# Optimization experiments

Measured on AMD Instinct MI355X. Metric: run time of the kernel, lower is better.

The kernel has to match this reference:

```python
import jax, jax.numpy as jnp
import numpy as np

B, T, F_IN, F_OUT = 16, 2048, 128, 128
ALPHA = 0.2  # LeakyReLU negative slope
MASK_VAL = -1e9


def setup_inputs() -> dict:
    key = jax.random.key(0)
    kx, kw, ka, kadj = jax.random.split(key, 4)
    # xavier_uniform-ish scale for W and a (gain=1.414)
    w_bound = 1.414 * np.sqrt(6.0 / (F_IN + F_OUT))
    a_bound = 1.414 * np.sqrt(6.0 / (2 * F_OUT + 1))
    x = jax.random.normal(kx, (B, T, F_IN), jnp.float32)
    W = jax.random.uniform(kw, (F_IN, F_OUT), jnp.float32, -w_bound, w_bound)
    a = jax.random.uniform(ka, (2 * F_OUT, 1), jnp.float32, -a_bound, a_bound)
    adj = jax.random.randint(kadj, (B, T, T), 0, 2, jnp.int32)
    return {"x": x, "adj": adj, "W": W, "a": a}


def reference(x, adj, W, a):
    # h: [B,T,F_OUT]
    h = jnp.einsum('btf,fo->bto', x, W)
    # Additive GAT score decomposition: e[b,i,j] = leakyrelu(h_i . a1 + h_j . a2)
    # Mathematically identical to cat([h_i,h_j]) @ a, without the BxTxTx2F tensor.
    a1 = a[:F_OUT, 0]   # [F_OUT]
    a2 = a[F_OUT:, 0]   # [F_OUT]
    s1 = h @ a1         # [B,T]
    s2 = h @ a2         # [B,T]
    e = jax.nn.leaky_relu(s1[:, :, None] + s2[:, None, :], ALPHA)  # [B,T,T]
    e = jnp.where(adj == 0, MASK_VAL, e)
    att = jax.nn.softmax(e, axis=-1)  # [B,T,T]
    # dropout=0.0 / eval mode -> identity
    return att @ h  # [B,T,F_OUT]
```

## Files before the change

kernel.cpp:

```cpp
#include <hip/hip_runtime.h>

#define TT 2048
#define NB 16
#define FD 128
#define ALPHA 0.2f

typedef __attribute__((ext_vector_type(8))) short short8;
typedef __attribute__((ext_vector_type(4))) float f32x4;

static __device__ __forceinline__ unsigned short f2bf(float f) {
    unsigned u = __float_as_uint(f);
    u += 0x7FFF + ((u >> 16) & 1);
    return (unsigned short)(u >> 16);
}
static __device__ __forceinline__ float bf2f(unsigned short s) {
    return __uint_as_float(((unsigned)s) << 16);
}

__global__ __launch_bounds__(256) void k_wt(const float* __restrict__ W,
                                            unsigned short* __restrict__ WT)
{
    int fid = blockIdx.x * 256 + threadIdx.x;
    int k = fid >> 5;
    int f = (fid & 31) << 2;
    float4 w4 = *reinterpret_cast<const float4*>(W + k * FD + f);
    WT[(f + 0) * FD + k] = f2bf(w4.x);
    WT[(f + 1) * FD + k] = f2bf(w4.y);
    WT[(f + 2) * FD + k] = f2bf(w4.z);
    WT[(f + 3) * FD + k] = f2bf(w4.w);
}

__global__ __launch_bounds__(256) void k_h(const float* __restrict__ x,
                                           const unsigned short* __restrict__ WT,
                                           const float* __restrict__ a,
                                           unsigned short* __restrict__ hT,
                                           float* __restrict__ s1,
                                           float* __restrict__ s2)
{
    __shared__ unsigned short hs[128][72];

    const int tid = threadIdx.x;
    const int b  = blockIdx.x >> 5;
    const int t0 = (blockIdx.x & 31) << 6;
    const int w = tid >> 6, l = tid & 63, g = l >> 4, r15 = l & 15;

    const float* xrow = x + ((size_t)(b * TT + t0 + w * 16 + r15)) * FD;

    f32x4 acc[8] = {};

    #pragma unroll
    for (int m = 0; m < 4; ++m) {
        const int koff = m * 32 + g * 8;
        float4 xa = *reinterpret_cast<const float4*>(xrow + koff);
        float4 xb = *reinterpret_cast<const float4*>(xrow + koff + 4);
        short8 af;
        af[0] = (short)f2bf(xa.x); af[1] = (short)f2bf(xa.y);
        af[2] = (short)f2bf(xa.z); af[3] = (short)f2bf(xa.w);
        af[4] = (short)f2bf(xb.x); af[5] = (short)f2bf(xb.y);
        af[6] = (short)f2bf(xb.z); af[7] = (short)f2bf(xb.w);
        #pragma unroll
        for (int n = 0; n < 8; ++n) {
            short8 bfr = *reinterpret_cast<const short8*>(WT + (n * 16 + r15) * FD + koff);
            acc[n] = __builtin_amdgcn_mfma_f32_16x16x32_bf16(af, bfr, acc[n], 0, 0, 0);
        }
    }

    float p1[4] = {0.f, 0.f, 0.f, 0.f}, p2[4] = {0.f, 0.f, 0.f, 0.f};
    #pragma unroll
    for (int n = 0; n < 8; ++n) {
        float a1v = a[n * 16 + r15];
        float a2v = a[FD + n * 16 + r15];
        #pragma unroll
        for (int r = 0; r < 4; ++r) {
            p1[r] += acc[n][r] * a1v;
            p2[r] += acc[n][r] * a2v;
        }
    }
    #pragma unroll
    for (int r = 0; r < 4; ++r) {
        #pragma unroll
        for (int off = 8; off >= 1; off >>= 1) {
            p1[r] += __shfl_xor(p1[r], off);
            p2[r] += __shfl_xor(p2[r], off);
        }
    }
    if (r15 == 0) {
        const int trow = t0 + w * 16 + g * 4;
        #pragma unroll
        for (int r = 0; r < 4; ++r) {
            s1[b * TT + trow + r] = p1[r];
            s2[b * TT + trow + r] = p2[r];
        }
    }

    #pragma unroll
    for (int n = 0; n < 8; ++n)
        #pragma unroll
        for (int r = 0; r < 4; ++r)
            hs[n * 16 + r15][w * 16 + g * 4 + r] = f2bf(acc[n][r]);
    __syncthreads();

    for (int i = tid; i < 1024; i += 256) {
        int f = i >> 3, c = i & 7;
        short8 v = *reinterpret_cast<const short8*>(&hs[f][c * 8]);
        *reinterpret_cast<short8*>(hT + ((size_t)(b * FD + f)) * TT + t0 + c * 8) = v;
    }
}

__global__ __launch_bounds__(256) void k_att(const int* __restrict__ adj,
                                             const unsigned short* __restrict__ hT,
                                             const float* __restrict__ s1,
                                             const float* __restrict__ s2,
                                             float* __restrict__ out)
{
    __shared__ __align__(16) unsigned short pbuf[2][32][136];
    __shared__ float dsum[32];

    const int tid = threadIdx.x;
    const int wg = (blockIdx.x & 7) * 128 + (blockIdx.x >> 3);
    const int b  = wg >> 6;
    const int i0 = (wg & 63) << 5;
    const int w = tid >> 6, l = tid & 63, g = l >> 4, r15 = l & 15;

    const int pr = tid >> 3;
    const int cg = tid & 7;
    const int* adjp = adj + ((size_t)(b * TT + i0 + pr)) * TT + cg * 16;
    const float s1v = s1[b * TT + i0 + pr];
    const float* s2p = s2 + b * TT + cg * 16;
    unsigned short* prow = &pbuf[0][pr][cg * 16];

    const int f0 = w * 32;
    const unsigned short* hB0 = hT + (size_t)b * FD * TT + (size_t)(f0 + r15) * TT;
    const unsigned short* hB1 = hB0 + (size_t)(16 * TT);

    f32x4 acc00 = {}, acc01 = {}, acc10 = {}, acc11 = {};
    float rsum = 0.f;

    int4 arA[4], arB[4];
    #pragma unroll
    for (int q = 0; q < 4; ++q)
        arA[q] = *reinterpret_cast<const int4*>(adjp + q * 4);

    auto body = [&](int t, int4 (&cur)[4], int4 (&nxt)[4], const int bsel) {
        const int j0 = t * 128;
        if (t < 15) {
            #pragma unroll
            for (int q = 0; q < 4; ++q)
                nxt[q] = *reinterpret_cast<const int4*>(adjp + j0 + 128 + q * 4);
        }
        float4 s2v[4];
        #pragma unroll
        for (int q = 0; q < 4; ++q)
            s2v[q] = *reinterpret_cast<const float4*>(s2p + j0 + q * 4);
        short8 v0, v1;
        const int*   cai = (const int*)cur;
        const float* csf = (const float*)s2v;
        #pragma unroll
        for (int e = 0; e < 16; ++e) {
            float s = s1v + csf[e];
            s = fmaxf(s, ALPHA * s);
            float p = cai[e] ? __expf(s) : 0.f;
            unsigned short u = f2bf(p);
            rsum += bf2f(u);
            if (e < 8) v0[e] = (short)u; else v1[e - 8] = (short)u;
        }
        unsigned short* dst = prow + bsel * (32 * 136);
        *reinterpret_cast<short8*>(dst)     = v0;
        *reinterpret_cast<short8*>(dst + 8) = v1;
        asm volatile("s_waitcnt lgkmcnt(0)" ::: "memory");
        __builtin_amdgcn_s_barrier();
        asm volatile("" ::: "memory");
        const unsigned short* pb = &pbuf[bsel][0][0];
        #pragma unroll
        for (int kk = 0; kk < 4; ++kk) {
            short8 A0 = *reinterpret_cast<const short8*>(pb + r15 * 136 + kk * 32 + g * 8);
            short8 A1 = *reinterpret_cast<const short8*>(pb + (16 + r15) * 136 + kk * 32 + g * 8);
            short8 B0 = *reinterpret_cast<const short8*>(hB0 + j0 + kk * 32 + g * 8);
            short8 B1 = *reinterpret_cast<const short8*>(hB1 + j0 + kk * 32 + g * 8);
            acc00 = __builtin_amdgcn_mfma_f32_16x16x32_bf16(A0, B0, acc00, 0, 0, 0);
            acc01 = __builtin_amdgcn_mfma_f32_16x16x32_bf16(A0, B1, acc01, 0, 0, 0);
            acc10 = __builtin_amdgcn_mfma_f32_16x16x32_bf16(A1, B0, acc10, 0, 0, 0);
            acc11 = __builtin_amdgcn_mfma_f32_16x16x32_bf16(A1, B1, acc11, 0, 0, 0);
        }
    };

    for (int tt = 0; tt < 8; ++tt) {
        body(2 * tt,     arA, arB, 0);
        body(2 * tt + 1, arB, arA, 1);
    }

    rsum += __shfl_xor(rsum, 1);
    rsum += __shfl_xor(rsum, 2);
    rsum += __shfl_xor(rsum, 4);
    if ((tid & 7) == 0) dsum[pr] = rsum;
    __syncthreads();

    float rinv0[4], rinv1[4];
    #pragma unroll
    for (int r = 0; r < 4; ++r) {
        rinv0[r] = 1.0f / dsum[g * 4 + r];
        rinv1[r] = 1.0f / dsum[16 + g * 4 + r];
    }
    const size_t obase = ((size_t)(b * TT + i0)) * FD + f0 + r15;
    #pragma unroll
    for (int r = 0; r < 4; ++r) {
        float* o0 = out + obase + (size_t)(g * 4 + r) * FD;
        float* o1 = out + obase + (size_t)(16 + g * 4 + r) * FD;
        o0[0]  = acc00[r] * rinv0[r];
        o0[16] = acc01[r] * rinv0[r];
        o1[0]  = acc10[r] * rinv1[r];
        o1[16] = acc11[r] * rinv1[r];
    }
}

extern "C" void kernel_launch(void* const* d_in, const int* in_sizes, int n_in,
                              void* d_out, int out_size, void* d_ws, size_t ws_size,
                              hipStream_t stream)
{
    const float* x  = (const float*)d_in[0];
    const int* adj  = (const int*)d_in[1];
    const float* W  = (const float*)d_in[2];
    const float* a  = (const float*)d_in[3];
    float* out = (float*)d_out;

    unsigned short* hT = (unsigned short*)d_ws;
    float* s1 = (float*)((char*)d_ws + (size_t)NB * FD * TT * 2);
    float* s2 = s1 + NB * TT;
    unsigned short* WT = (unsigned short*)(s2 + NB * TT);

    k_wt <<<16, 256, 0, stream>>>(W, WT);
    k_h  <<<NB * (TT / 64), 256, 0, stream>>>(x, WT, a, hT, s1, s2);
    k_att<<<NB * (TT / 32), 256, 0, stream>>>(adj, hT, s1, s2, out);
}
```

Before: 123.4 us.

## Shrink attention row tile from 32 to 16 rows to double block count

The attention kernel now handles 16 query rows per block instead of 32, launching twice as many blocks with half the accumulators and half the shared-memory P buffer, and adds an occupancy hint of 8 blocks per CU. Each thread computes 8 probabilities per 128-column step instead of 16. This is meant to raise parallelism and occupancy so the adjacency stream, which dominates traffic, is fetched with more memory-level parallelism. The cost is that the hT tile is read from global/L2 twice as many times in total, and MFMA work per barrier is halved.

```diff
diff --git a/kernel.cpp b/kernel.cpp
--- a/kernel.cpp
+++ b/kernel.cpp
@@ -107,66 +107,60 @@
     }
 }
 
-__global__ __launch_bounds__(256) void k_att(const int* __restrict__ adj,
-                                             const unsigned short* __restrict__ hT,
-                                             const float* __restrict__ s1,
-                                             const float* __restrict__ s2,
-                                             float* __restrict__ out)
-{
-    __shared__ __align__(16) unsigned short pbuf[2][32][136];
-    __shared__ float dsum[32];
+__global__ __launch_bounds__(256, 8) void k_att(const int* __restrict__ adj,
+                                                const unsigned short* __restrict__ hT,
+                                                const float* __restrict__ s1,
+                                                const float* __restrict__ s2,
+                                                float* __restrict__ out)
+{
+    __shared__ __align__(16) unsigned short pbuf[2][16][136];
+    __shared__ float dsum[16];
 
     const int tid = threadIdx.x;
-    const int wg = (blockIdx.x & 7) * 128 + (blockIdx.x >> 3);
-    const int b  = wg >> 6;
-    const int i0 = (wg & 63) << 5;
+    const int wg = (blockIdx.x & 7) * 256 + (blockIdx.x >> 3);
+    const int b  = wg >> 7;
+    const int i0 = (wg & 127) << 4;
     const int w = tid >> 6, l = tid & 63, g = l >> 4, r15 = l & 15;
 
-    const int pr = tid >> 3;
-    const int cg = tid & 7;
-    const int* adjp = adj + ((size_t)(b * TT + i0 + pr)) * TT + cg * 16;
+    const int pr = tid >> 4;
+    const int cg = tid & 15;
+    const int* adjp = adj + ((size_t)(b * TT + i0 + pr)) * TT + cg * 8;
     const float s1v = s1[b * TT + i0 + pr];
-    const float* s2p = s2 + b * TT + cg * 16;
-    unsigned short* prow = &pbuf[0][pr][cg * 16];
+    const float* s2p = s2 + b * TT + cg * 8;
+    unsigned short* prow = &pbuf[0][pr][cg * 8];
 
     const int f0 = w * 32;
     const unsigned short* hB0 = hT + (size_t)b * FD * TT + (size_t)(f0 + r15) * TT;
     const unsigned short* hB1 = hB0 + (size_t)(16 * TT);
 
-    f32x4 acc00 = {}, acc01 = {}, acc10 = {}, acc11 = {};
+    f32x4 acc0 = {}, acc1 = {};
     float rsum = 0.f;
 
-    int4 arA[4], arB[4];
-    #pragma unroll
-    for (int q = 0; q < 4; ++q)
-        arA[q] = *reinterpret_cast<const int4*>(adjp + q * 4);
-
-    auto body = [&](int t, int4 (&cur)[4], int4 (&nxt)[4], const int bsel) {
+    int4 arA[2], arB[2];
+    arA[0] = *reinterpret_cast<const int4*>(adjp);
+    arA[1] = *reinterpret_cast<const int4*>(adjp + 4);
+
+    auto body = [&](int t, int4 (&cur)[2], int4 (&nxt)[2], const int bsel) {
         const int j0 = t * 128;
         if (t < 15) {
-            #pragma unroll
-            for (int q = 0; q < 4; ++q)
-                nxt[q] = *reinterpret_cast<const int4*>(adjp + j0 + 128 + q * 4);
-        }
-        float4 s2v[4];
-        #pragma unroll
-        for (int q = 0; q < 4; ++q)
-            s2v[q] = *reinterpret_cast<const float4*>(s2p + j0 + q * 4);
-        short8 v0, v1;
-        const int*   cai = (const int*)cur;
-        const float* csf = (const float*)s2v;
-        #pragma unroll
-        for (int e = 0; e < 16; ++e) {
+            nxt[0] = *reinterpret_cast<const int4*>(adjp + j0 + 128);
+            nxt[1] = *reinterpret_cast<const int4*>(adjp + j0 + 132);
+        }
+        float4 s2a = *reinterpret_cast<const float4*>(s2p + j0);
+        float4 s2b = *reinterpret_cast<const float4*>(s2p + j0 + 4);
+        short8 v0;
+        const int* cai = (const int*)cur;
+        float csf[8] = {s2a.x, s2a.y, s2a.z, s2a.w, s2b.x, s2b.y, s2b.z, s2b.w};
+        #pragma unroll
+        for (int e = 0; e < 8; ++e) {
             float s = s1v + csf[e];
             s = fmaxf(s, ALPHA * s);
             float p = cai[e] ? __expf(s) : 0.f;
             unsigned short u = f2bf(p);
             rsum += bf2f(u);
-            if (e < 8) v0[e] = (short)u; else v1[e - 8] = (short)u;
-        }
-        unsigned short* dst = prow + bsel * (32 * 136);
-        *reinterpret_cast<short8*>(dst)     = v0;
-        *reinterpret_cast<short8*>(dst + 8) = v1;
+            v0[e] = (short)u;
+        }
+        *reinterpret_cast<short8*>(prow + bsel * (16 * 136)) = v0;
         asm volatile("s_waitcnt lgkmcnt(0)" ::: "memory");
         __builtin_amdgcn_s_barrier();
         asm volatile("" ::: "memory");
@@ -174,13 +168,10 @@
         #pragma unroll
         for (int kk = 0; kk < 4; ++kk) {
             short8 A0 = *reinterpret_cast<const short8*>(pb + r15 * 136 + kk * 32 + g * 8);
-            short8 A1 = *reinterpret_cast<const short8*>(pb + (16 + r15) * 136 + kk * 32 + g * 8);
             short8 B0 = *reinterpret_cast<const short8*>(hB0 + j0 + kk * 32 + g * 8);
             short8 B1 = *reinterpret_cast<const short8*>(hB1 + j0 + kk * 32 + g * 8);
-            acc00 = __builtin_amdgcn_mfma_f32_16x16x32_bf16(A0, B0, acc00, 0, 0, 0);
-            acc01 = __builtin_amdgcn_mfma_f32_16x16x32_bf16(A0, B1, acc01, 0, 0, 0);
-            acc10 = __builtin_amdgcn_mfma_f32_16x16x32_bf16(A1, B0, acc10, 0, 0, 0);
-            acc11 = __builtin_amdgcn_mfma_f32_16x16x32_bf16(A1, B1, acc11, 0, 0, 0);
+            acc0 = __builtin_amdgcn_mfma_f32_16x16x32_bf16(A0, B0, acc0, 0, 0, 0);
+            acc1 = __builtin_amdgcn_mfma_f32_16x16x32_bf16(A0, B1, acc1, 0, 0, 0);
         }
     };
 
@@ -192,24 +183,20 @@
     rsum += __shfl_xor(rsum, 1);
     rsum += __shfl_xor(rsum, 2);
     rsum += __shfl_xor(rsum, 4);
-    if ((tid & 7) == 0) dsum[pr] = rsum;
+    rsum += __shfl_xor(rsum, 8);
+    if ((tid & 15) == 0) dsum[pr] = rsum;
     __syncthreads();
 
-    float rinv0[4], rinv1[4];
+    float rinv[4];
+    #pragma unroll
+    for (int r = 0; r < 4; ++r) rinv[r] = 1.0f / dsum[g * 4 + r];
+
+    const size_t obase = ((size_t)(b * TT + i0)) * FD + f0 + r15;
     #pragma unroll
     for (int r = 0; r < 4; ++r) {
-        rinv0[r] = 1.0f / dsum[g * 4 + r];
-        rinv1[r] = 1.0f / dsum[16 + g * 4 + r];
-    }
-    const size_t obase = ((size_t)(b * TT + i0)) * FD + f0 + r15;
-    #pragma unroll
-    for (int r = 0; r < 4; ++r) {
-        float* o0 = out + obase + (size_t)(g * 4 + r) * FD;
-        float* o1 = out + obase + (size_t)(16 + g * 4 + r) * FD;
-        o0[0]  = acc00[r] * rinv0[r];
-        o0[16] = acc01[r] * rinv0[r];
-        o1[0]  = acc10[r] * rinv1[r];
-        o1[16] = acc11[r] * rinv1[r];
+        float* o = out + obase + (size_t)(g * 4 + r) * FD;
+        o[0]  = acc0[r] * rinv[r];
+        o[16] = acc1[r] * rinv[r];
     }
 }
 
@@ -230,5 +217,5 @@
 
     k_wt <<<16, 256, 0, stream>>>(W, WT);
     k_h  <<<NB * (TT / 64), 256, 0, stream>>>(x, WT, a, hT, s1, s2);
-    k_att<<<NB * (TT / 32), 256, 0, stream>>>(adj, hT, s1, s2, out);
-}
+    k_att<<<NB * (TT / 16), 256, 0, stream>>>(adj, hT, s1, s2, out);
+}
```

Result: slower. 174.9 us (+41.7%).
